# Kernel tuning notes

Hardware: AMD Instinct MI355X
Metric: run time of the kernel (lower is better)

Reference implementation:

```python
import jax, jax.numpy as jnp
import numpy as np

CAM_THRESHOLD = 0.1
ITERATIONS = 5
EPS = 1e-8


def _region_growing(cam_maps, normed_features, labels):
    # cam_maps: [B,C,H,W]; normed_features: [B,D,H,W]; labels: [B,C] int
    B, C, H, W = cam_maps.shape
    dt = cam_maps.dtype
    refined = (cam_maps > CAM_THRESHOLD).astype(dt)
    label_ok = labels > 0  # [B,C]
    for it in range(ITERATIONS):
        fg = (refined > 0.5).astype(dt)                      # [B,C,H,W]
        fg_count = fg.sum(axis=(2, 3))                       # [B,C]
        active = (fg_count > 0) & label_ok                   # skip empty / absent classes
        # per-(b,c) mean foreground feature, then cosine similarity map
        fg_sum = jnp.einsum('bdhw,bchw->bcd', normed_features, fg)
        fg_mean = fg_sum / (fg_count[..., None] + EPS)       # [B,C,D]
        sim = jnp.einsum('bdhw,bcd->bchw', normed_features, fg_mean)
        strictness = 0.5 - 0.05 * it
        thr = sim.mean(axis=(2, 3)) + strictness * jnp.std(sim, axis=(2, 3), ddof=1)
        thr4 = thr[..., None, None]                          # [B,C,1,1]
        new_px = (sim > thr4) & ~(fg > 0.5)
        if it > 0:
            # 3x3 ones-conv dilation == 3x3 max window on a {0,1} mask
            dil = jax.lax.reduce_window(fg, 0.0, jax.lax.max,
                                        (1, 1, 3, 3), (1, 1, 1, 1), 'SAME') > 0
            new_px = new_px & dil
        conf = (sim - thr4) / (sim.max(axis=(2, 3), keepdims=True) - thr4 + EPS)
        conf = jnp.clip(conf, 0.1, 0.9)
        add = jnp.where(new_px, conf, jnp.zeros((), dt)) * active[..., None, None].astype(dt)
        refined = refined + add
    refined = jnp.clip(refined, 0.0, 1.0)
    max_idx = jnp.argmax(refined, axis=1)                    # [B,H,W], first-max like torch
    one_hot = jax.nn.one_hot(max_idx, C, axis=1, dtype=dt)
    return refined * one_hot


def reference(cam_raw, proj_w, proj_b, labels):
    cam = jax.nn.relu(cam_raw)                               # cam = relu(unet(x))
    pooled = cam.mean(axis=(2, 3))                           # GAP -> logits [B,C]
    # 1x1 conv feature projection: [B,C,H,W] -> [B,64,H,W]
    feat = jnp.einsum('bchw,dc->bdhw', cam, proj_w) + proj_b[None, :, None, None]
    norm = jnp.linalg.norm(feat, axis=1, keepdims=True)
    normed = feat / (norm + EPS)
    seg = _region_growing(cam, normed, labels)
    return pooled, seg


def setup_inputs() -> dict:
    key = jax.random.key(0)
    k1, k2, k3, k4 = jax.random.split(key, 4)
    B, C, H, W, D = 8, 21, 256, 256, 64
    cam_raw = jax.random.normal(k1, (B, C, H, W), dtype=jnp.float32)
    proj_w = jax.random.normal(k2, (D, C), dtype=jnp.float32) * 0.1
    proj_b = jax.random.normal(k3, (D,), dtype=jnp.float32) * 0.01
    labels = jax.random.randint(k4, (B, C), 0, 2, dtype=jnp.int32)
    return {'cam_raw': cam_raw, 'proj_w': proj_w, 'proj_b': proj_b, 'labels': labels}
```

## Files before the change

kernel.cpp:

```cpp
#include <hip/hip_runtime.h>

#define B 8
#define C 21
#define H 256
#define W 256
#define HW 65536
#define D 64
#define NPIX (B*HW)
#define EPSF 1e-8f
#define FG_CH 4

__device__ __forceinline__ unsigned enc_max(float v) {
    unsigned u = __float_as_uint(v);
    return (v >= 0.f) ? (u | 0x80000000u) : ~u;
}
__device__ __forceinline__ float dec_max(unsigned k) {
    return (k & 0x80000000u) ? __uint_as_float(k & 0x7fffffffu) : __uint_as_float(~k);
}

__global__ void k_zero(double* fg_sum, double* st1, double* st2, unsigned* stm,
                       int* cnt0, int* cnt1, double* pooled_acc) {
    int tid = threadIdx.x;
    for (int i = tid; i < B * C * D; i += 256) fg_sum[i] = 0.0;
    if (tid < B * C) {
        st1[tid] = 0.0; st2[tid] = 0.0; stm[tid] = 0u;
        cnt0[tid] = 0; cnt1[tid] = 0; pooled_acc[tid] = 0.0;
    }
}

__global__ __launch_bounds__(256, 2)
void k_feat(const float* __restrict__ cam_raw,
            const float* __restrict__ proj_w,
            const float* __restrict__ proj_b,
            float* __restrict__ normed,
            float* __restrict__ refined,
            unsigned* __restrict__ fb0,
            int* __restrict__ cnt0,
            double* __restrict__ pooled_acc) {
    __shared__ float pw[D * C];
    __shared__ float pb[D];
    __shared__ double wp[4][C];
    __shared__ int wc[4][C];
    for (int i = threadIdx.x; i < D * C; i += 256) pw[i] = proj_w[i];
    if (threadIdx.x < D) pb[threadIdx.x] = proj_b[threadIdx.x];
    __syncthreads();
    int gid = blockIdx.x * 256 + threadIdx.x;
    int b = gid >> 16, pix = gid & 65535;
    int lane = threadIdx.x & 63, wv = threadIdx.x >> 6;
    float cam[C];
    unsigned m = 0;
    #pragma unroll
    for (int c = 0; c < C; ++c) {
        float v = cam_raw[((size_t)(b * C + c)) * HW + pix];
        v = v > 0.f ? v : 0.f;
        cam[c] = v;
        refined[((size_t)(b * C + c)) * HW + pix] = (v > 0.1f) ? 1.f : 0.f;
        m |= (v > 0.1f ? 1u : 0u) << c;
    }
    fb0[(size_t)b * HW + pix] = m;
    float feat[D];
    float ss = 0.f;
    #pragma unroll
    for (int d = 0; d < D; ++d) {
        float f = pb[d];
        #pragma unroll
        for (int c = 0; c < C; ++c) f = fmaf(pw[d * C + c], cam[c], f);
        feat[d] = f;
        ss = fmaf(f, f, ss);
    }
    float nrm = sqrtf(ss) + EPSF;
    #pragma unroll
    for (int d = 0; d < D; ++d)
        normed[((size_t)(b * D + d)) * HW + pix] = feat[d] / nrm;
    #pragma unroll
    for (int c = 0; c < C; ++c) {
        unsigned long long bl = __ballot((m >> c) & 1u);
        if (lane == 0) wc[wv][c] = (int)__popcll(bl);
    }
    #pragma unroll
    for (int c = 0; c < C; ++c) {
        double s = (double)cam[c];
        #pragma unroll
        for (int o = 32; o > 0; o >>= 1) s += __shfl_xor(s, o);
        if (lane == 0) wp[wv][c] = s;
    }
    __syncthreads();
    if (threadIdx.x < C) {
        int c = threadIdx.x;
        atomicAdd(&cnt0[b * C + c], wc[0][c] + wc[1][c] + wc[2][c] + wc[3][c]);
        atomicAdd(&pooled_acc[b * C + c], wp[0][c] + wp[1][c] + wp[2][c] + wp[3][c]);
    }
}

__global__ __launch_bounds__(256, 4)
void k_fgsum(const float* __restrict__ normed,
             const unsigned* __restrict__ fb,
             double* __restrict__ fg_sum) {
    int bd = blockIdx.y;
    int b = bd >> 6, d = bd & 63;
    int seg = blockIdx.x;
    const float* nf = normed + ((size_t)(b * D + d)) * HW + seg * (HW / FG_CH);
    const unsigned* mb = fb + (size_t)b * HW + seg * (HW / FG_CH);
    float acc[C];
    #pragma unroll
    for (int c = 0; c < C; ++c) acc[c] = 0.f;
    for (int p = 0; p < HW / FG_CH; p += 1024) {
        int off = p + threadIdx.x * 4;
        float4 v = *reinterpret_cast<const float4*>(nf + off);
        uint4 m = *reinterpret_cast<const uint4*>(mb + off);
        #pragma unroll
        for (int c = 0; c < C; ++c) {
            acc[c] = fmaf((float)((m.x >> c) & 1u), v.x, acc[c]);
            acc[c] = fmaf((float)((m.y >> c) & 1u), v.y, acc[c]);
            acc[c] = fmaf((float)((m.z >> c) & 1u), v.z, acc[c]);
            acc[c] = fmaf((float)((m.w >> c) & 1u), v.w, acc[c]);
        }
    }
    int lane = threadIdx.x & 63;
    #pragma unroll
    for (int c = 0; c < C; ++c) {
        double s = (double)acc[c];
        #pragma unroll
        for (int o = 32; o > 0; o >>= 1) s += __shfl_xor(s, o);
        if (lane == 0) atomicAdd(&fg_sum[((size_t)(b * C + c)) * D + d], s);
    }
}

__global__ void k_fgmean(const double* __restrict__ fg_sum,
                         const int* __restrict__ cnt,
                         float* __restrict__ fg_mean,
                         const double* __restrict__ pooled_acc,
                         float* __restrict__ pooled, int first) {
    int i = blockIdx.x * 256 + threadIdx.x;
    if (i < B * C * D) {
        int bc = i / D;
        fg_mean[i] = (float)(fg_sum[i] / ((double)cnt[bc] + 1e-8));
    }
    if (first && i < B * C) pooled[i] = (float)(pooled_acc[i] / 65536.0);
}

__global__ __launch_bounds__(256, 2)
void k_sim(const float* __restrict__ normed,
           const float* __restrict__ fg_mean,
           float* __restrict__ sim,
           double* __restrict__ st1, double* __restrict__ st2,
           unsigned* __restrict__ stm) {
    int b = blockIdx.y;
    __shared__ float fm[C * D];
    __shared__ double w1[4][C], w2[4][C];
    __shared__ float wm[4][C];
    for (int i = threadIdx.x; i < C * D; i += 256) fm[i] = fg_mean[b * C * D + i];
    __syncthreads();
    int pix4 = (blockIdx.x * 256 + threadIdx.x) * 4;
    int lane = threadIdx.x & 63, wv = threadIdx.x >> 6;
    const float* nb = normed + (size_t)b * D * HW + pix4;
    float4 acc[C];
    #pragma unroll
    for (int c = 0; c < C; ++c) acc[c] = make_float4(0.f, 0.f, 0.f, 0.f);
    for (int d0 = 0; d0 < D; d0 += 4) {
        float4 v0 = *reinterpret_cast<const float4*>(nb + (size_t)(d0 + 0) * HW);
        float4 v1 = *reinterpret_cast<const float4*>(nb + (size_t)(d0 + 1) * HW);
        float4 v2 = *reinterpret_cast<const float4*>(nb + (size_t)(d0 + 2) * HW);
        float4 v3 = *reinterpret_cast<const float4*>(nb + (size_t)(d0 + 3) * HW);
        #pragma unroll
        for (int c = 0; c < C; ++c) {
            float4 f = *reinterpret_cast<const float4*>(&fm[c * D + d0]);
            acc[c].x = fmaf(v0.x, f.x, acc[c].x); acc[c].y = fmaf(v0.y, f.x, acc[c].y);
            acc[c].z = fmaf(v0.z, f.x, acc[c].z); acc[c].w = fmaf(v0.w, f.x, acc[c].w);
            acc[c].x = fmaf(v1.x, f.y, acc[c].x); acc[c].y = fmaf(v1.y, f.y, acc[c].y);
            acc[c].z = fmaf(v1.z, f.y, acc[c].z); acc[c].w = fmaf(v1.w, f.y, acc[c].w);
            acc[c].x = fmaf(v2.x, f.z, acc[c].x); acc[c].y = fmaf(v2.y, f.z, acc[c].y);
            acc[c].z = fmaf(v2.z, f.z, acc[c].z); acc[c].w = fmaf(v2.w, f.z, acc[c].w);
            acc[c].x = fmaf(v3.x, f.w, acc[c].x); acc[c].y = fmaf(v3.y, f.w, acc[c].y);
            acc[c].z = fmaf(v3.z, f.w, acc[c].z); acc[c].w = fmaf(v3.w, f.w, acc[c].w);
        }
    }
    #pragma unroll
    for (int c = 0; c < C; ++c)
        *reinterpret_cast<float4*>(sim + ((size_t)(b * C + c)) * HW + pix4) = acc[c];
    #pragma unroll
    for (int c = 0; c < C; ++c) {
        double x = acc[c].x, y = acc[c].y, z = acc[c].z, w = acc[c].w;
        double s1 = x + y + z + w;
        double s2 = x * x + y * y + z * z + w * w;
        float mx = fmaxf(fmaxf(acc[c].x, acc[c].y), fmaxf(acc[c].z, acc[c].w));
        #pragma unroll
        for (int o = 32; o > 0; o >>= 1) {
            s1 += __shfl_xor(s1, o);
            s2 += __shfl_xor(s2, o);
            mx = fmaxf(mx, __shfl_xor(mx, o));
        }
        if (lane == 0) { w1[wv][c] = s1; w2[wv][c] = s2; wm[wv][c] = mx; }
    }
    __syncthreads();
    if (threadIdx.x < C) {
        int c = threadIdx.x;
        double s1 = w1[0][c] + w1[1][c] + w1[2][c] + w1[3][c];
        double s2 = w2[0][c] + w2[1][c] + w2[2][c] + w2[3][c];
        float mx = fmaxf(fmaxf(wm[0][c], wm[1][c]), fmaxf(wm[2][c], wm[3][c]));
        atomicAdd(&st1[b * C + c], s1);
        atomicAdd(&st2[b * C + c], s2);
        atomicMax(&stm[b * C + c], enc_max(mx));
    }
}

__global__ void k_thr(double* __restrict__ st1, double* __restrict__ st2,
                      unsigned* __restrict__ stm,
                      const int* __restrict__ cnt_cur, const int* __restrict__ labels,
                      float* __restrict__ thr_arr, float* __restrict__ den_arr,
                      float* __restrict__ act_arr, float strict,
                      double* __restrict__ fg_sum, int* __restrict__ cnt_nxt) {
    int bc = threadIdx.x;
    if (bc < B * C) {
        double n = 65536.0;
        double s1 = st1[bc], s2 = st2[bc];
        double mean = s1 / n;
        double var = (s2 - s1 * s1 / n) / (n - 1.0);
        if (var < 0.0) var = 0.0;
        float t = (float)(mean + (double)strict * sqrt(var));
        float mx = dec_max(stm[bc]);
        thr_arr[bc] = t;
        den_arr[bc] = mx - t + EPSF;
        act_arr[bc] = (cnt_cur[bc] > 0 && labels[bc] > 0) ? 1.f : 0.f;
        st1[bc] = 0.0; st2[bc] = 0.0; stm[bc] = 0u; cnt_nxt[bc] = 0;
    }
    for (int i = threadIdx.x; i < B * C * D; i += 256) fg_sum[i] = 0.0;
}

__global__ void k_update(const float* __restrict__ sim,
                         const unsigned* __restrict__ fbc,
                         unsigned* __restrict__ fbn,
                         const float* __restrict__ thr_arr, const float* __restrict__ den_arr,
                         const float* __restrict__ act_arr,
                         float* __restrict__ refined, int* __restrict__ cnt_nxt, int it) {
    int b = blockIdx.y;
    int t = blockIdx.x * 256 + threadIdx.x;
    int pix4 = t * 4;
    int h = pix4 >> 8, w = pix4 & 255;
    int lane = threadIdx.x & 63, wv = threadIdx.x >> 6;
    const unsigned* fb = fbc + (size_t)b * HW;
    uint4 msv = *reinterpret_cast<const uint4*>(fb + pix4);
    unsigned ms[4] = {msv.x, msv.y, msv.z, msv.w};
    unsigned dil[4];
    if (it > 0) {
        unsigned up[6], mi[6], dn[6];
        bool hm = h > 0, hp = h < H - 1;
        #pragma unroll
        for (int j = 0; j < 6; ++j) {
            int ww = w - 1 + j;
            bool okw = (ww >= 0) && (ww < W);
            mi[j] = okw ? fb[h * W + ww] : 0u;
            up[j] = (okw && hm) ? fb[(h - 1) * W + ww] : 0u;
            dn[j] = (okw && hp) ? fb[(h + 1) * W + ww] : 0u;
        }
        #pragma unroll
        for (int j = 0; j < 4; ++j)
            dil[j] = up[j] | up[j+1] | up[j+2] | mi[j] | mi[j+1] | mi[j+2]
                   | dn[j] | dn[j+1] | dn[j+2];
    } else {
        #pragma unroll
        for (int j = 0; j < 4; ++j) dil[j] = 0xFFFFFFFFu;
    }
    unsigned nm[4] = {0u, 0u, 0u, 0u};
    int cnt[C];
    #pragma unroll
    for (int c = 0; c < C; ++c) cnt[c] = 0;
    #pragma unroll
    for (int c = 0; c < C; ++c) {
        int bc = b * C + c;
        float thr = thr_arr[bc], den = den_arr[bc], act = act_arr[bc];
        size_t idx = (size_t)bc * HW + pix4;
        float4 s4 = *reinterpret_cast<const float4*>(sim + idx);
        float4 r4 = *reinterpret_cast<float4*>(refined + idx);
        float sv[4] = {s4.x, s4.y, s4.z, s4.w};
        float rv[4] = {r4.x, r4.y, r4.z, r4.w};
        bool changed = false;
        #pragma unroll
        for (int j = 0; j < 4; ++j) {
            bool fg = (ms[j] >> c) & 1u;
            bool npx = (sv[j] > thr) && !fg && ((dil[j] >> c) & 1u);
            if (npx && act > 0.f) {
                float conf = (sv[j] - thr) / den;
                conf = fminf(fmaxf(conf, 0.1f), 0.9f);
                rv[j] += conf;
                changed = true;
            }
            unsigned nb = (rv[j] > 0.5f) ? 1u : 0u;
            nm[j] |= nb << c;
            cnt[c] += (int)nb;
        }
        if (changed) {
            float4 o4 = make_float4(rv[0], rv[1], rv[2], rv[3]);
            *reinterpret_cast<float4*>(refined + idx) = o4;
        }
    }
    uint4 nmv = make_uint4(nm[0], nm[1], nm[2], nm[3]);
    *reinterpret_cast<uint4*>(fbn + (size_t)b * HW + pix4) = nmv;
    __shared__ int wc[4][C];
    #pragma unroll
    for (int c = 0; c < C; ++c) {
        int v = cnt[c];
        #pragma unroll
        for (int o = 32; o > 0; o >>= 1) v += __shfl_xor(v, o);
        if (lane == 0) wc[wv][c] = v;
    }
    __syncthreads();
    if (threadIdx.x < C) {
        int c = threadIdx.x;
        atomicAdd(&cnt_nxt[b * C + c], wc[0][c] + wc[1][c] + wc[2][c] + wc[3][c]);
    }
}

__global__ __launch_bounds__(256, 2)
void k_final(float* __restrict__ refined) {
    int b = blockIdx.y;
    int pix4 = (blockIdx.x * 256 + threadIdx.x) * 4;
    float4 vals[C];
    #pragma unroll
    for (int c = 0; c < C; ++c) {
        float4 v = *reinterpret_cast<const float4*>(refined + ((size_t)(b * C + c)) * HW + pix4);
        v.x = fminf(fmaxf(v.x, 0.f), 1.f);
        v.y = fminf(fmaxf(v.y, 0.f), 1.f);
        v.z = fminf(fmaxf(v.z, 0.f), 1.f);
        v.w = fminf(fmaxf(v.w, 0.f), 1.f);
        vals[c] = v;
    }
    int bi[4] = {0, 0, 0, 0};
    float bv[4] = {vals[0].x, vals[0].y, vals[0].z, vals[0].w};
    #pragma unroll
    for (int c = 1; c < C; ++c) {
        float vv[4] = {vals[c].x, vals[c].y, vals[c].z, vals[c].w};
        #pragma unroll
        for (int j = 0; j < 4; ++j)
            if (vv[j] > bv[j]) { bv[j] = vv[j]; bi[j] = c; }
    }
    #pragma unroll
    for (int c = 0; c < C; ++c) {
        float4 v = vals[c];
        float4 o;
        o.x = (bi[0] == c) ? v.x : 0.f;
        o.y = (bi[1] == c) ? v.y : 0.f;
        o.z = (bi[2] == c) ? v.z : 0.f;
        o.w = (bi[3] == c) ? v.w : 0.f;
        *reinterpret_cast<float4*>(refined + ((size_t)(b * C + c)) * HW + pix4) = o;
    }
}

extern "C" void kernel_launch(void* const* d_in, const int* in_sizes, int n_in,
                              void* d_out, int out_size, void* d_ws, size_t ws_size,
                              hipStream_t stream) {
    const float* cam_raw = (const float*)d_in[0];
    const float* proj_w  = (const float*)d_in[1];
    const float* proj_b  = (const float*)d_in[2];
    const int*   labels  = (const int*)d_in[3];
    float* out = (float*)d_out;
    float* pooled  = out;
    float* refined = out + B * C;

    char* ws = (char*)d_ws;
    float* normed = (float*)ws;          ws += (size_t)B * D * HW * 4;
    float* sim    = (float*)ws;          ws += (size_t)B * C * HW * 4;
    unsigned* fb0 = (unsigned*)ws;       ws += (size_t)B * HW * 4;
    unsigned* fb1 = (unsigned*)ws;       ws += (size_t)B * HW * 4;
    double* fg_sum = (double*)ws;        ws += (size_t)B * C * D * 8;
    double* st1    = (double*)ws;        ws += (size_t)B * C * 8;
    double* st2    = (double*)ws;        ws += (size_t)B * C * 8;
    double* pooled_acc = (double*)ws;    ws += (size_t)B * C * 8;
    unsigned* stm  = (unsigned*)ws;      ws += (size_t)B * C * 4;
    int* cnt0      = (int*)ws;           ws += (size_t)B * C * 4;
    int* cnt1      = (int*)ws;           ws += (size_t)B * C * 4;
    float* fg_mean = (float*)ws;         ws += (size_t)B * C * D * 4;
    float* thr_arr = (float*)ws;         ws += (size_t)B * C * 4;
    float* den_arr = (float*)ws;         ws += (size_t)B * C * 4;
    float* act_arr = (float*)ws;         ws += (size_t)B * C * 4;
    unsigned* fbs[2] = {fb0, fb1};
    int* cnts[2] = {cnt0, cnt1};

    hipLaunchKernelGGL(k_zero, dim3(1), dim3(256), 0, stream,
                       fg_sum, st1, st2, stm, cnt0, cnt1, pooled_acc);
    hipLaunchKernelGGL(k_feat, dim3(NPIX / 256), dim3(256), 0, stream,
                       cam_raw, proj_w, proj_b, normed, refined, fb0, cnt0, pooled_acc);
    for (int it = 0; it < 5; ++it) {
        int cur = it & 1, nxt = cur ^ 1;
        hipLaunchKernelGGL(k_fgsum, dim3(FG_CH, B * D), dim3(256), 0, stream,
                           normed, fbs[cur], fg_sum);
        hipLaunchKernelGGL(k_fgmean, dim3((B * C * D + 255) / 256), dim3(256), 0, stream,
                           fg_sum, cnts[cur], fg_mean, pooled_acc, pooled, it == 0 ? 1 : 0);
        hipLaunchKernelGGL(k_sim, dim3(HW / 1024, B), dim3(256), 0, stream,
                           normed, fg_mean, sim, st1, st2, stm);
        float strict = (float)(0.5 - 0.05 * (double)it);
        hipLaunchKernelGGL(k_thr, dim3(1), dim3(256), 0, stream,
                           st1, st2, stm, cnts[cur], labels,
                           thr_arr, den_arr, act_arr, strict, fg_sum, cnts[nxt]);
        hipLaunchKernelGGL(k_update, dim3(HW / 1024, B), dim3(256), 0, stream,
                           sim, fbs[cur], fbs[nxt], thr_arr, den_arr, act_arr,
                           refined, cnts[nxt], it);
    }
    hipLaunchKernelGGL(k_final, dim3(HW / 1024, B), dim3(256), 0, stream, refined);
}
```

Baseline: 958.3 us.

## Vectorize feature kernel to 4 pixels per thread and fold fg-mean into sim

k_feat now handles four pixels per thread with float4 loads and stores. It recomputes the 64-channel projection in a second pass instead of keeping a feat array in registers, and raises the launch-bounds occupancy hint. The separate fg_mean kernel is removed: k_sim computes the mean from fg_sum and counts while loading shared memory, and writes pooled on the first pass. k_thr spreads the fg_sum zeroing across 8 blocks. This trades extra FMA work in k_feat for fewer registers and wider memory transactions, and drops five kernel launches.

Result: slower. 1.293 ms (+34.9%).

```diff
diff --git a/kernel.cpp b/kernel.cpp
--- a/kernel.cpp
+++ b/kernel.cpp
@@ -28,7 +28,7 @@
     }
 }
 
-__global__ __launch_bounds__(256, 2)
+__global__ __launch_bounds__(256, 4)
 void k_feat(const float* __restrict__ cam_raw,
             const float* __restrict__ proj_w,
             const float* __restrict__ proj_b,
@@ -45,41 +45,68 @@
     if (threadIdx.x < D) pb[threadIdx.x] = proj_b[threadIdx.x];
     __syncthreads();
     int gid = blockIdx.x * 256 + threadIdx.x;
-    int b = gid >> 16, pix = gid & 65535;
+    int b = gid >> 14;
+    int pix4 = (gid << 2) & 65535;
     int lane = threadIdx.x & 63, wv = threadIdx.x >> 6;
-    float cam[C];
-    unsigned m = 0;
-    #pragma unroll
-    for (int c = 0; c < C; ++c) {
-        float v = cam_raw[((size_t)(b * C + c)) * HW + pix];
-        v = v > 0.f ? v : 0.f;
+    float4 cam[C];
+    unsigned m0 = 0, m1 = 0, m2 = 0, m3 = 0;
+    #pragma unroll
+    for (int c = 0; c < C; ++c) {
+        float4 v = *reinterpret_cast<const float4*>(cam_raw + ((size_t)(b * C + c)) * HW + pix4);
+        v.x = v.x > 0.f ? v.x : 0.f;
+        v.y = v.y > 0.f ? v.y : 0.f;
+        v.z = v.z > 0.f ? v.z : 0.f;
+        v.w = v.w > 0.f ? v.w : 0.f;
         cam[c] = v;
-        refined[((size_t)(b * C + c)) * HW + pix] = (v > 0.1f) ? 1.f : 0.f;
-        m |= (v > 0.1f ? 1u : 0u) << c;
-    }
-    fb0[(size_t)b * HW + pix] = m;
-    float feat[D];
-    float ss = 0.f;
-    #pragma unroll
+        unsigned b0 = v.x > 0.1f ? 1u : 0u, b1 = v.y > 0.1f ? 1u : 0u;
+        unsigned b2 = v.z > 0.1f ? 1u : 0u, b3 = v.w > 0.1f ? 1u : 0u;
+        m0 |= b0 << c; m1 |= b1 << c; m2 |= b2 << c; m3 |= b3 << c;
+        float4 r = make_float4((float)b0, (float)b1, (float)b2, (float)b3);
+        *reinterpret_cast<float4*>(refined + ((size_t)(b * C + c)) * HW + pix4) = r;
+    }
+    *reinterpret_cast<uint4*>(fb0 + (size_t)b * HW + pix4) = make_uint4(m0, m1, m2, m3);
+    float sx = 0.f, sy = 0.f, sz = 0.f, sw = 0.f;
     for (int d = 0; d < D; ++d) {
-        float f = pb[d];
-        #pragma unroll
-        for (int c = 0; c < C; ++c) f = fmaf(pw[d * C + c], cam[c], f);
-        feat[d] = f;
-        ss = fmaf(f, f, ss);
-    }
-    float nrm = sqrtf(ss) + EPSF;
-    #pragma unroll
-    for (int d = 0; d < D; ++d)
-        normed[((size_t)(b * D + d)) * HW + pix] = feat[d] / nrm;
-    #pragma unroll
-    for (int c = 0; c < C; ++c) {
-        unsigned long long bl = __ballot((m >> c) & 1u);
-        if (lane == 0) wc[wv][c] = (int)__popcll(bl);
-    }
-    #pragma unroll
-    for (int c = 0; c < C; ++c) {
-        double s = (double)cam[c];
+        float fx = pb[d], fy = fx, fz = fx, fw = fx;
+        #pragma unroll
+        for (int c = 0; c < C; ++c) {
+            float ww = pw[d * C + c];
+            fx = fmaf(ww, cam[c].x, fx);
+            fy = fmaf(ww, cam[c].y, fy);
+            fz = fmaf(ww, cam[c].z, fz);
+            fw = fmaf(ww, cam[c].w, fw);
+        }
+        sx = fmaf(fx, fx, sx); sy = fmaf(fy, fy, sy);
+        sz = fmaf(fz, fz, sz); sw = fmaf(fw, fw, sw);
+    }
+    float ix = 1.f / (sqrtf(sx) + EPSF);
+    float iy = 1.f / (sqrtf(sy) + EPSF);
+    float iz = 1.f / (sqrtf(sz) + EPSF);
+    float iw = 1.f / (sqrtf(sw) + EPSF);
+    for (int d = 0; d < D; ++d) {
+        float fx = pb[d], fy = fx, fz = fx, fw = fx;
+        #pragma unroll
+        for (int c = 0; c < C; ++c) {
+            float ww = pw[d * C + c];
+            fx = fmaf(ww, cam[c].x, fx);
+            fy = fmaf(ww, cam[c].y, fy);
+            fz = fmaf(ww, cam[c].z, fz);
+            fw = fmaf(ww, cam[c].w, fw);
+        }
+        float4 o = make_float4(fx * ix, fy * iy, fz * iz, fw * iw);
+        *reinterpret_cast<float4*>(normed + ((size_t)(b * D + d)) * HW + pix4) = o;
+    }
+    #pragma unroll
+    for (int c = 0; c < C; ++c) {
+        int v = (int)((m0 >> c) & 1u) + (int)((m1 >> c) & 1u)
+              + (int)((m2 >> c) & 1u) + (int)((m3 >> c) & 1u);
+        #pragma unroll
+        for (int o = 32; o > 0; o >>= 1) v += __shfl_xor(v, o);
+        if (lane == 0) wc[wv][c] = v;
+    }
+    #pragma unroll
+    for (int c = 0; c < C; ++c) {
+        double s = (double)cam[c].x + (double)cam[c].y + (double)cam[c].z + (double)cam[c].w;
         #pragma unroll
         for (int o = 32; o > 0; o >>= 1) s += __shfl_xor(s, o);
         if (lane == 0) wp[wv][c] = s;
@@ -126,30 +153,25 @@
     }
 }
 
-__global__ void k_fgmean(const double* __restrict__ fg_sum,
-                         const int* __restrict__ cnt,
-                         float* __restrict__ fg_mean,
-                         const double* __restrict__ pooled_acc,
-                         float* __restrict__ pooled, int first) {
-    int i = blockIdx.x * 256 + threadIdx.x;
-    if (i < B * C * D) {
-        int bc = i / D;
-        fg_mean[i] = (float)(fg_sum[i] / ((double)cnt[bc] + 1e-8));
-    }
-    if (first && i < B * C) pooled[i] = (float)(pooled_acc[i] / 65536.0);
-}
-
 __global__ __launch_bounds__(256, 2)
 void k_sim(const float* __restrict__ normed,
-           const float* __restrict__ fg_mean,
+           const double* __restrict__ fg_sum,
+           const int* __restrict__ cnt,
            float* __restrict__ sim,
            double* __restrict__ st1, double* __restrict__ st2,
-           unsigned* __restrict__ stm) {
+           unsigned* __restrict__ stm,
+           const double* __restrict__ pooled_acc,
+           float* __restrict__ pooled, int first) {
     int b = blockIdx.y;
     __shared__ float fm[C * D];
     __shared__ double w1[4][C], w2[4][C];
     __shared__ float wm[4][C];
-    for (int i = threadIdx.x; i < C * D; i += 256) fm[i] = fg_mean[b * C * D + i];
+    for (int i = threadIdx.x; i < C * D; i += 256) {
+        int c = i / D;
+        fm[i] = (float)(fg_sum[(size_t)b * C * D + i] / ((double)cnt[b * C + c] + 1e-8));
+    }
+    if (first && blockIdx.x == 0 && threadIdx.x < B * C)
+        pooled[threadIdx.x] = (float)(pooled_acc[threadIdx.x] / 65536.0);
     __syncthreads();
     int pix4 = (blockIdx.x * 256 + threadIdx.x) * 4;
     int lane = threadIdx.x & 63, wv = threadIdx.x >> 6;
@@ -210,21 +232,25 @@
                       float* __restrict__ thr_arr, float* __restrict__ den_arr,
                       float* __restrict__ act_arr, float strict,
                       double* __restrict__ fg_sum, int* __restrict__ cnt_nxt) {
-    int bc = threadIdx.x;
-    if (bc < B * C) {
-        double n = 65536.0;
-        double s1 = st1[bc], s2 = st2[bc];
-        double mean = s1 / n;
-        double var = (s2 - s1 * s1 / n) / (n - 1.0);
-        if (var < 0.0) var = 0.0;
-        float t = (float)(mean + (double)strict * sqrt(var));
-        float mx = dec_max(stm[bc]);
-        thr_arr[bc] = t;
-        den_arr[bc] = mx - t + EPSF;
-        act_arr[bc] = (cnt_cur[bc] > 0 && labels[bc] > 0) ? 1.f : 0.f;
-        st1[bc] = 0.0; st2[bc] = 0.0; stm[bc] = 0u; cnt_nxt[bc] = 0;
-    }
-    for (int i = threadIdx.x; i < B * C * D; i += 256) fg_sum[i] = 0.0;
+    const int slice = B * C * D / 8;
+    int base = blockIdx.x * slice;
+    for (int i = threadIdx.x; i < slice; i += 256) fg_sum[base + i] = 0.0;
+    if (blockIdx.x == 0) {
+        int bc = threadIdx.x;
+        if (bc < B * C) {
+            double n = 65536.0;
+            double s1 = st1[bc], s2 = st2[bc];
+            double mean = s1 / n;
+            double var = (s2 - s1 * s1 / n) / (n - 1.0);
+            if (var < 0.0) var = 0.0;
+            float t = (float)(mean + (double)strict * sqrt(var));
+            float mx = dec_max(stm[bc]);
+            thr_arr[bc] = t;
+            den_arr[bc] = mx - t + EPSF;
+            act_arr[bc] = (cnt_cur[bc] > 0 && labels[bc] > 0) ? 1.f : 0.f;
+            st1[bc] = 0.0; st2[bc] = 0.0; stm[bc] = 0u; cnt_nxt[bc] = 0;
+        }
+    }
 }
 
 __global__ void k_update(const float* __restrict__ sim,
@@ -369,7 +395,6 @@
     unsigned* stm  = (unsigned*)ws;      ws += (size_t)B * C * 4;
     int* cnt0      = (int*)ws;           ws += (size_t)B * C * 4;
     int* cnt1      = (int*)ws;           ws += (size_t)B * C * 4;
-    float* fg_mean = (float*)ws;         ws += (size_t)B * C * D * 4;
     float* thr_arr = (float*)ws;         ws += (size_t)B * C * 4;
     float* den_arr = (float*)ws;         ws += (size_t)B * C * 4;
     float* act_arr = (float*)ws;         ws += (size_t)B * C * 4;
@@ -378,18 +403,17 @@
 
     hipLaunchKernelGGL(k_zero, dim3(1), dim3(256), 0, stream,
                        fg_sum, st1, st2, stm, cnt0, cnt1, pooled_acc);
-    hipLaunchKernelGGL(k_feat, dim3(NPIX / 256), dim3(256), 0, stream,
+    hipLaunchKernelGGL(k_feat, dim3(NPIX / 1024), dim3(256), 0, stream,
                        cam_raw, proj_w, proj_b, normed, refined, fb0, cnt0, pooled_acc);
     for (int it = 0; it < 5; ++it) {
         int cur = it & 1, nxt = cur ^ 1;
         hipLaunchKernelGGL(k_fgsum, dim3(FG_CH, B * D), dim3(256), 0, stream,
                            normed, fbs[cur], fg_sum);
-        hipLaunchKernelGGL(k_fgmean, dim3((B * C * D + 255) / 256), dim3(256), 0, stream,
-                           fg_sum, cnts[cur], fg_mean, pooled_acc, pooled, it == 0 ? 1 : 0);
         hipLaunchKernelGGL(k_sim, dim3(HW / 1024, B), dim3(256), 0, stream,
-                           normed, fg_mean, sim, st1, st2, stm);
+                           normed, fg_sum, cnts[cur], sim, st1, st2, stm,
+                           pooled_acc, pooled, it == 0 ? 1 : 0);
         float strict = (float)(0.5 - 0.05 * (double)it);
-        hipLaunchKernelGGL(k_thr, dim3(1), dim3(256), 0, stream,
+        hipLaunchKernelGGL(k_thr, dim3(8), dim3(256), 0, stream,
                            st1, st2, stm, cnts[cur], labels,
                            thr_arr, den_arr, act_arr, strict, fg_sum, cnts[nxt]);
         hipLaunchKernelGGL(k_update, dim3(HW / 1024, B), dim3(256), 0, stream,
```
